# Optimization experiments

Measured on AMD Instinct MI355X. Metric: run time of the kernel, lower is better.

Reference implementation:

```python
import jax, jax.numpy as jnp
import numpy as np

B, NQ, NC, D, H = 4, 4096, 4096, 1024, 16
HD = D // H
LN_EPS = 1e-5


def _layernorm(x, g, b):
    mu = jnp.mean(x, axis=-1, keepdims=True)
    var = jnp.var(x, axis=-1, keepdims=True)
    return (x - mu) * jax.lax.rsqrt(var + LN_EPS) * g + b


def _kernel(x):
    # elu(x) + 1  (strictly positive feature map)
    return jax.nn.elu(x) + 1.0


def setup_inputs() -> dict:
    key = jax.random.key(0)
    ks = jax.random.split(key, 12)
    s = 1.0 / np.sqrt(D)
    return {
        "query": jax.random.normal(ks[0], (B, NQ, D), jnp.float32),
        "context": jax.random.normal(ks[1], (B, NC, D), jnp.float32),
        "q_w": jax.random.uniform(ks[2], (D, D), jnp.float32, -s, s),
        "q_b": jnp.zeros((D,), jnp.float32),
        "k_w": jax.random.uniform(ks[3], (D, D), jnp.float32, -s, s),
        "k_b": jnp.zeros((D,), jnp.float32),
        "v_w": jax.random.uniform(ks[4], (D, D), jnp.float32, -s, s),
        "v_b": jnp.zeros((D,), jnp.float32),
        "o_w": jax.random.uniform(ks[5], (D, D), jnp.float32, -s, s),
        "o_b": jnp.zeros((D,), jnp.float32),
        "lnq_g": jnp.ones((D,), jnp.float32),
        "lnq_b": jnp.zeros((D,), jnp.float32),
        "lnkv_g": jnp.ones((D,), jnp.float32),
        "lnkv_b": jnp.zeros((D,), jnp.float32),
    }


def reference(query, context, q_w, q_b, k_w, k_b, v_w, v_b, o_w, o_b,
              lnq_g, lnq_b, lnkv_g, lnkv_b):
    residual = query
    q = _layernorm(query, lnq_g, lnq_b)
    c = _layernorm(context, lnkv_g, lnkv_b)

    # torch Linear: y = x @ W.T + b ; reshape to (B, H, N, Hd)
    Q = (q @ q_w.T + q_b).reshape(B, NQ, H, HD).transpose(0, 2, 1, 3)
    K = (c @ k_w.T + k_b).reshape(B, NC, H, HD).transpose(0, 2, 1, 3)
    V = (c @ v_w.T + v_b).reshape(B, NC, H, HD).transpose(0, 2, 1, 3)

    Q = _kernel(Q)
    K = _kernel(K)

    # KV: (B, H, Hd, Hd) outer-product accumulation over context length
    KV = jnp.einsum("bhnd,bhne->bhde", K, V)
    K_sum = K.sum(axis=2)                              # (B, H, Hd)
    Z = jnp.einsum("bhqd,bhd->bhq", Q, K_sum)          # (B, H, Nq)
    Z = jnp.maximum(Z, 1e-6)

    out = jnp.einsum("bhqd,bhde->bhqe", Q, KV) / Z[..., None]
    out = out.transpose(0, 2, 1, 3).reshape(B, NQ, D)
    return residual + (out @ o_w.T + o_b)
```

## Files before the change

### kernel.cpp

```cpp
#include <hip/hip_runtime.h>

#define DEV __device__ __forceinline__

typedef __attribute__((ext_vector_type(8))) short short8;
typedef __attribute__((ext_vector_type(4))) short short4v;
typedef __attribute__((ext_vector_type(4))) float f32x4;

DEV float bf2f(unsigned short u) { return __uint_as_float(((unsigned int)u) << 16); }
DEV unsigned short f2bf(float f) {
    unsigned int u = __float_as_uint(f);
    u += 0x7FFFu + ((u >> 16) & 1u);
    return (unsigned short)(u >> 16);
}

DEV float elu1(float v) { return v > 0.0f ? v + 1.0f : __expf(v); }

DEV void gload_lds16(const void* g, void* l) {
    __builtin_amdgcn_global_load_lds(
        (__attribute__((address_space(1))) unsigned int*)(g),
        (__attribute__((address_space(3))) unsigned int*)(l),
        16, 0, 0);
}

#define NROW 16384
#define DDIM 1024

__global__ __launch_bounds__(256) void ln_kernel(
    const float* __restrict__ query, const float* __restrict__ context,
    const float* __restrict__ lnq_g, const float* __restrict__ lnq_b,
    const float* __restrict__ lnk_g, const float* __restrict__ lnk_b,
    unsigned short* __restrict__ qln, unsigned short* __restrict__ cln)
{
    const int row = blockIdx.x;
    const bool isq = row < NROW;
    const int r = isq ? row : row - NROW;
    const float* src = (isq ? query : context) + (size_t)r * DDIM;
    const float* g   = isq ? lnq_g : lnk_g;
    const float* bb  = isq ? lnq_b : lnk_b;
    unsigned short* dst = (isq ? qln : cln) + (size_t)r * DDIM;

    const int tid = threadIdx.x;
    f32x4 x = *(const f32x4*)(src + tid * 4);
    float s  = x[0] + x[1] + x[2] + x[3];
    float sq = x[0]*x[0] + x[1]*x[1] + x[2]*x[2] + x[3]*x[3];
#pragma unroll
    for (int off = 32; off; off >>= 1) {
        s  += __shfl_xor(s, off);
        sq += __shfl_xor(sq, off);
    }
    __shared__ float red[8];
    const int lane = tid & 63, w = tid >> 6;
    if (lane == 0) { red[w] = s; red[4 + w] = sq; }
    __syncthreads();
    s  = red[0] + red[1] + red[2] + red[3];
    sq = red[4] + red[5] + red[6] + red[7];
    const float mu  = s * (1.0f / DDIM);
    const float var = sq * (1.0f / DDIM) - mu * mu;
    const float rstd = rsqrtf(var + 1e-5f);

    f32x4 gv = *(const f32x4*)(g + tid * 4);
    f32x4 bv = *(const f32x4*)(bb + tid * 4);
    short4v o;
#pragma unroll
    for (int j = 0; j < 4; ++j)
        o[j] = (short)f2bf((x[j] - mu) * rstd * gv[j] + bv[j]);
    *(short4v*)(dst + tid * 4) = o;
}

__global__ __launch_bounds__(256) void conv_w(
    const float* __restrict__ a, const float* __restrict__ b,
    const float* __restrict__ c, const float* __restrict__ d,
    unsigned short* __restrict__ out)
{
    const int i = blockIdx.x * 256 + threadIdx.x;
    const int mat = i >> 18;
    const int idx = (i & 262143) * 4;
    const float* src = mat == 0 ? a : mat == 1 ? b : mat == 2 ? c : d;
    f32x4 v = *(const f32x4*)(src + idx);
    short4v o;
#pragma unroll
    for (int j = 0; j < 4; ++j) o[j] = (short)f2bf(v[j]);
    *(short4v*)(out + (size_t)mat * 1048576 + idx) = o;
}

template <typename EPI>
DEV void gemm128(unsigned short* __restrict__ sA,
                 unsigned short* __restrict__ sB,
                 const unsigned short* __restrict__ Ap,
                 const unsigned short* __restrict__ Bp,
                 int m0, int n0, EPI epi)
{
    const int tid = threadIdx.x;
    const int lane = tid & 63, w = tid >> 6;
    const int wr = w >> 1, wc = w & 1;
    const int lr = lane & 15, lg = lane >> 4;

    const int srow = tid >> 3;
    const int cswz = (tid & 7) ^ (srow & 7);
    const unsigned short* gA0 = Ap + (size_t)(m0 + srow) * 1024 + cswz * 8;
    const unsigned short* gB0 = Bp + (size_t)(n0 + srow) * 1024 + cswz * 8;
    unsigned short* dA = sA + tid * 8;
    unsigned short* dB = sB + tid * 8;

    const int sw0 = ((0 + lg) ^ (lr & 7)) * 8;
    const int sw1 = ((4 + lg) ^ (lr & 7)) * 8;

    f32x4 acc[4][4];
#pragma unroll
    for (int i = 0; i < 4; ++i)
#pragma unroll
        for (int j = 0; j < 4; ++j)
#pragma unroll
            for (int e = 0; e < 4; ++e) acc[i][j][e] = 0.0f;

#define STG8(T)                                                               \
    {                                                                         \
        const int ko = (T) * 64;                                              \
        _Pragma("unroll")                                                     \
        for (int j = 0; j < 4; ++j) {                                         \
            gload_lds16(gA0 + ko + (size_t)j * 32768, dA + j * 2048);         \
            gload_lds16(gB0 + ko + (size_t)j * 32768, dB + j * 2048);         \
        }                                                                     \
    }

    STG8(0);
    for (int t = 0; t < 16; ++t) {
        asm volatile("s_waitcnt vmcnt(0)" ::: "memory");
        __builtin_amdgcn_s_barrier();

        short8 af[4], bf[4];
#pragma unroll
        for (int mt = 0; mt < 4; ++mt)
            af[mt] = *(const short8*)&sA[(wr * 64 + mt * 16 + lr) * 64 + sw0];
#pragma unroll
        for (int nt = 0; nt < 4; ++nt)
            bf[nt] = *(const short8*)&sB[(wc * 64 + nt * 16 + lr) * 64 + sw0];
        __builtin_amdgcn_s_setprio(1);
#pragma unroll
        for (int mt = 0; mt < 4; ++mt)
#pragma unroll
            for (int nt = 0; nt < 4; ++nt)
                acc[mt][nt] = __builtin_amdgcn_mfma_f32_16x16x32_bf16(
                    af[mt], bf[nt], acc[mt][nt], 0, 0, 0);
        __builtin_amdgcn_s_setprio(0);

#pragma unroll
        for (int mt = 0; mt < 4; ++mt)
            af[mt] = *(const short8*)&sA[(wr * 64 + mt * 16 + lr) * 64 + sw1];
#pragma unroll
        for (int nt = 0; nt < 4; ++nt)
            bf[nt] = *(const short8*)&sB[(wc * 64 + nt * 16 + lr) * 64 + sw1];
        asm volatile("s_waitcnt lgkmcnt(0)" ::: "memory");
        __builtin_amdgcn_s_barrier();
        if (t < 15) STG8(t + 1);
        __builtin_amdgcn_s_setprio(1);
#pragma unroll
        for (int mt = 0; mt < 4; ++mt)
#pragma unroll
            for (int nt = 0; nt < 4; ++nt)
                acc[mt][nt] = __builtin_amdgcn_mfma_f32_16x16x32_bf16(
                    af[mt], bf[nt], acc[mt][nt], 0, 0, 0);
        __builtin_amdgcn_s_setprio(0);
    }
#undef STG8

#pragma unroll
    for (int mt = 0; mt < 4; ++mt)
#pragma unroll
        for (int nt = 0; nt < 4; ++nt) {
            const int col = n0 + wc * 64 + nt * 16 + lr;
#pragma unroll
            for (int i = 0; i < 4; ++i) {
                const int row = m0 + wr * 64 + mt * 16 + lg * 4 + i;
                epi(row, col, acc[mt][nt][i]);
            }
        }
}

__global__ __launch_bounds__(256, 4) void gemm_qkv(
    const unsigned short* __restrict__ QLN, const unsigned short* __restrict__ WQ,
    const unsigned short* __restrict__ CLN, const unsigned short* __restrict__ WKV,
    unsigned short* __restrict__ Qm, unsigned short* __restrict__ KVT,
    const float* __restrict__ q_b, const float* __restrict__ k_b,
    const float* __restrict__ v_b)
{
    __shared__ __attribute__((aligned(16))) unsigned short sA[128 * 64];
    __shared__ __attribute__((aligned(16))) unsigned short sB[128 * 64];

    const int bid = blockIdx.x;
    const int l = (bid & 7) * 384 + (bid >> 3);

    if (l < 1024) {
        const int m0 = (l >> 3) * 128, n0 = (l & 7) * 128;
        gemm128(sA, sB, QLN, WQ, m0, n0,
            [&](int row, int col, float v) {
                v = elu1(v + q_b[col]);
                Qm[(size_t)row * 1024 + col] = f2bf(v);
            });
    } else {
        const int r = l - 1024;
        const int m0 = (r & 15) * 128, n0 = (r >> 4) * 128;
        gemm128(sA, sB, WKV, CLN, m0, n0,
            [&](int row, int col, float v) {
                if (row < 1024) v = elu1(v + k_b[row]);
                else            v = v + v_b[row - 1024];
                KVT[(size_t)row * NROW + col] = f2bf(v);
            });
    }
}

__global__ __launch_bounds__(512, 2) void gemm_out256(
    const unsigned short* __restrict__ A, const unsigned short* __restrict__ Bm,
    float* __restrict__ Cout, const float* __restrict__ bias,
    const float* __restrict__ resid)
{
    __shared__ __attribute__((aligned(16))) unsigned short smem[65536];
    unsigned short* sAb = smem;
    unsigned short* sBb = smem + 32768;

    const int bid = blockIdx.x;
    const int l = (bid & 7) * 32 + (bid >> 3);
    const int m0 = (l >> 2) * 256, n0 = (l & 3) * 256;

    const int tid = threadIdx.x;
    const int lane = tid & 63, w = tid >> 6;
    const int wr = w >> 2, wc = w & 3;
    const int lr = lane & 15, lg = lane >> 4;

    const int srow = tid >> 3;
    const int cswz = (tid & 7) ^ (srow & 7);
    const unsigned short* gA0 = A  + (size_t)(m0 + srow) * 1024 + cswz * 8;
    const unsigned short* gB0 = Bm + (size_t)(n0 + srow) * 1024 + cswz * 8;

    const int sw0 = ((0 + lg) ^ (lr & 7)) * 8;
    const int sw1 = ((4 + lg) ^ (lr & 7)) * 8;

    f32x4 acc[8][4];
#pragma unroll
    for (int i = 0; i < 8; ++i)
#pragma unroll
        for (int j = 0; j < 4; ++j)
#pragma unroll
            for (int e = 0; e < 4; ++e) acc[i][j][e] = 0.0f;

#define STG(GP, SP, T)                                                        \
    {                                                                         \
        const unsigned short* g = (GP) + (T) * 64;                            \
        unsigned short* d = (SP) + ((T) & 1) * 16384 + tid * 8;               \
        _Pragma("unroll")                                                     \
        for (int L = 0; L < 4; ++L)                                           \
            gload_lds16(g + (size_t)L * 65536, d + L * 4096);                 \
    }

    STG(gB0, sBb, 0); STG(gA0, sAb, 0); STG(gB0, sBb, 1); STG(gA0, sAb, 1);
    asm volatile("s_waitcnt vmcnt(8)" ::: "memory");
    __builtin_amdgcn_s_barrier();

    short8 bvl[2][2];
#pragma unroll
    for (int nt = 0; nt < 2; ++nt) {
        const int rb = (wc * 64 + nt * 16 + lr) * 64;
        bvl[nt][0] = *(const short8*)&sBb[rb + sw0];
        bvl[nt][1] = *(const short8*)&sBb[rb + sw1];
    }

    for (int t = 0; t < 16; ++t) {
        const unsigned short* bA = sAb + (t & 1) * 16384;
        const unsigned short* bB = sBb + (t & 1) * 16384;
        const unsigned short* bBn = sBb + ((t + 1) & 1) * 16384;
        short8 afl[4][2], afh[4][2], bvh[2][2], bvln[2][2];

#pragma unroll
        for (int mt = 0; mt < 4; ++mt) {
            const int ra = (wr * 128 + mt * 16 + lr) * 64;
            afl[mt][0] = *(const short8*)&bA[ra + sw0];
            afl[mt][1] = *(const short8*)&bA[ra + sw1];
        }
#pragma unroll
        for (int mt = 0; mt < 4; ++mt) {
            const int ra = (wr * 128 + (mt + 4) * 16 + lr) * 64;
            afh[mt][0] = *(const short8*)&bA[ra + sw0];
            afh[mt][1] = *(const short8*)&bA[ra + sw1];
        }
        asm volatile("s_waitcnt lgkmcnt(8)" ::: "memory");
        __builtin_amdgcn_s_setprio(1);
#pragma unroll
        for (int kk = 0; kk < 2; ++kk)
#pragma unroll
            for (int mt = 0; mt < 4; ++mt)
#pragma unroll
                for (int nt = 0; nt < 2; ++nt)
                    acc[mt][nt] = __builtin_amdgcn_mfma_f32_16x16x32_bf16(
                        afl[mt][kk], bvl[nt][kk], acc[mt][nt], 0, 0, 0);
        __builtin_amdgcn_s_setprio(0);
        __builtin_amdgcn_s_barrier();

#pragma unroll
        for (int nt = 0; nt < 2; ++nt) {
            const int rb = (wc * 64 + (nt + 2) * 16 + lr) * 64;
            bvh[nt][0] = *(const short8*)&bB[rb + sw0];
            bvh[nt][1] = *(const short8*)&bB[rb + sw1];
        }
        asm volatile("s_waitcnt lgkmcnt(4)" ::: "memory");
        __builtin_amdgcn_s_setprio(1);
#pragma unroll
        for (int kk = 0; kk < 2; ++kk)
#pragma unroll
            for (int mt = 0; mt < 4; ++mt)
#pragma unroll
                for (int nt = 0; nt < 2; ++nt)
                    acc[mt + 4][nt] = __builtin_amdgcn_mfma_f32_16x16x32_bf16(
                        afh[mt][kk], bvl[nt][kk], acc[mt + 4][nt], 0, 0, 0);
        __builtin_amdgcn_s_setprio(0);
        asm volatile("s_waitcnt vmcnt(0)" ::: "memory");
        __builtin_amdgcn_s_barrier();

        if (t < 15) {
#pragma unroll
            for (int nt = 0; nt < 2; ++nt) {
                const int rb = (wc * 64 + nt * 16 + lr) * 64;
                bvln[nt][0] = *(const short8*)&bBn[rb + sw0];
                bvln[nt][1] = *(const short8*)&bBn[rb + sw1];
            }
        }
        if (t + 2 < 16) STG(gA0, sAb, t + 2);
        if (t < 15) asm volatile("s_waitcnt lgkmcnt(4)" ::: "memory");
        else        asm volatile("s_waitcnt lgkmcnt(0)" ::: "memory");
        __builtin_amdgcn_s_setprio(1);
#pragma unroll
        for (int kk = 0; kk < 2; ++kk)
#pragma unroll
            for (int mt = 0; mt < 4; ++mt)
#pragma unroll
                for (int nt = 0; nt < 2; ++nt)
                    acc[mt + 4][nt + 2] = __builtin_amdgcn_mfma_f32_16x16x32_bf16(
                        afh[mt][kk], bvh[nt][kk], acc[mt + 4][nt + 2], 0, 0, 0);
        __builtin_amdgcn_s_setprio(0);
        __builtin_amdgcn_s_barrier();

        if (t + 2 < 16) STG(gB0, sBb, t + 2);
        __builtin_amdgcn_s_setprio(1);
#pragma unroll
        for (int kk = 0; kk < 2; ++kk)
#pragma unroll
            for (int mt = 0; mt < 4; ++mt)
#pragma unroll
                for (int nt = 0; nt < 2; ++nt)
                    acc[mt][nt + 2] = __builtin_amdgcn_mfma_f32_16x16x32_bf16(
                        afl[mt][kk], bvh[nt][kk], acc[mt][nt + 2], 0, 0, 0);
        __builtin_amdgcn_s_setprio(0);

        if (t < 15) {
#pragma unroll
            for (int nt = 0; nt < 2; ++nt) {
                bvl[nt][0] = bvln[nt][0];
                bvl[nt][1] = bvln[nt][1];
            }
        }
    }
#undef STG

#pragma unroll
    for (int mt = 0; mt < 8; ++mt) {
#pragma unroll
        for (int nt = 0; nt < 4; ++nt) {
            const int col = n0 + wc * 64 + nt * 16 + lr;
#pragma unroll
            for (int i = 0; i < 4; ++i) {
                const int row = m0 + wr * 128 + mt * 16 + lg * 4 + i;
                Cout[(size_t)row * 1024 + col] =
                    acc[mt][nt][i] + bias[col] + resid[(size_t)row * 1024 + col];
            }
        }
    }
}

__global__ __launch_bounds__(256) void kv_kernel(
    const unsigned short* __restrict__ VT, const unsigned short* __restrict__ KT,
    float* __restrict__ KVTp, float* __restrict__ Ksump)
{
    const int bh = blockIdx.x, sp = blockIdx.y;
    const int b = bh >> 4, h = bh & 15;
    const int tid = threadIdx.x, lane = tid & 63, w = tid >> 6;
    const int lr = lane & 15, lg = lane >> 4;

    f32x4 acc[4][4];
#pragma unroll
    for (int i = 0; i < 4; ++i)
#pragma unroll
        for (int j = 0; j < 4; ++j)
#pragma unroll
            for (int e = 0; e < 4; ++e) acc[i][j][e] = 0.0f;
    float kp[4] = {0.0f, 0.0f, 0.0f, 0.0f};

    const size_t colbase = (size_t)b * 4096 + sp * 1024 + w * 256 + lg * 8;
    const unsigned short* va = VT + (size_t)(h * 64 + lr) * NROW + colbase;
    const unsigned short* ka = KT + (size_t)(h * 64 + lr) * NROW + colbase;

    for (int ks = 0; ks < 8; ++ks) {
        short8 af[4], bfv[4];
#pragma unroll
        for (int mt = 0; mt < 4; ++mt)
            af[mt] = *(const short8*)(va + (size_t)mt * 16 * NROW + ks * 32);
#pragma unroll
        for (int nt = 0; nt < 4; ++nt)
            bfv[nt] = *(const short8*)(ka + (size_t)nt * 16 * NROW + ks * 32);
#pragma unroll
        for (int mt = 0; mt < 4; ++mt)
#pragma unroll
            for (int nt = 0; nt < 4; ++nt)
                acc[mt][nt] = __builtin_amdgcn_mfma_f32_16x16x32_bf16(
                    af[mt], bfv[nt], acc[mt][nt], 0, 0, 0);
#pragma unroll
        for (int nt = 0; nt < 4; ++nt)
#pragma unroll
            for (int j = 0; j < 8; ++j)
                kp[nt] += bf2f((unsigned short)bfv[nt][j]);
    }

#pragma unroll
    for (int nt = 0; nt < 4; ++nt) {
        kp[nt] += __shfl_xor(kp[nt], 16);
        kp[nt] += __shfl_xor(kp[nt], 32);
    }
    __shared__ float kred[4][64];
    if (lane < 16) {
#pragma unroll
        for (int nt = 0; nt < 4; ++nt) kred[w][nt * 16 + lane] = kp[nt];
    }

    __shared__ float red4[4][4096];
#pragma unroll
    for (int mt = 0; mt < 4; ++mt)
#pragma unroll
        for (int nt = 0; nt < 4; ++nt)
#pragma unroll
            for (int i = 0; i < 4; ++i)
                red4[w][(mt * 16 + lg * 4 + i) * 64 + nt * 16 + lr] = acc[mt][nt][i];
    __syncthreads();
    float* out = KVTp + ((size_t)sp * 64 + bh) * 4096;
    for (int i = tid; i < 4096; i += 256)
        out[i] = red4[0][i] + red4[1][i] + red4[2][i] + red4[3][i];
    if (tid < 64)
        Ksump[((size_t)sp * 64 + bh) * 64 + tid] =
            kred[0][tid] + kred[1][tid] + kred[2][tid] + kred[3][tid];
}

__global__ __launch_bounds__(256) void z_kernel(
    const unsigned short* __restrict__ Q, const float* __restrict__ Ksump,
    float* __restrict__ invZ)
{
    const int gid = blockIdx.x * 256 + threadIdx.x;
    const int n = gid >> 4, h = gid & 15;
    const int b = n >> 12;
    const unsigned short* q = Q + (size_t)n * DDIM + h * 64;
    const float* k0 = Ksump + ((size_t)((b << 4) + h)) * 64;
    float z = 0.0f;
#pragma unroll
    for (int it = 0; it < 8; ++it) {
        short8 v = *(const short8*)(q + it * 8);
#pragma unroll
        for (int j = 0; j < 8; ++j) {
            const int d = it * 8 + j;
            const float ksv = k0[d] + k0[d + 4096] + k0[d + 8192] + k0[d + 12288];
            z += bf2f((unsigned short)v[j]) * ksv;
        }
    }
    invZ[gid] = 1.0f / fmaxf(z, 1e-6f);
}

__global__ __launch_bounds__(256) void a2_kernel(
    const unsigned short* __restrict__ Q, const float* __restrict__ KVTp,
    const float* __restrict__ invZ, unsigned short* __restrict__ A2)
{
    const int m0 = blockIdx.x * 128, h = blockIdx.y;
    const int b = m0 >> 12, bh = (b << 4) + h;
    const int tid = threadIdx.x, lane = tid & 63, w = tid >> 6;
    const int wr = w >> 1, wc = w & 1;
    const int lr = lane & 15, lg = lane >> 4;

    f32x4 acc[4][2];
#pragma unroll
    for (int i = 0; i < 4; ++i)
#pragma unroll
        for (int j = 0; j < 2; ++j)
#pragma unroll
            for (int e = 0; e < 4; ++e) acc[i][j][e] = 0.0f;

    const unsigned short* qa = Q + (size_t)(m0 + wr * 64 + lr) * DDIM + h * 64 + lg * 8;
    const float* kvb = KVTp + (size_t)bh * 4096 + (wc * 32 + lr) * 64 + lg * 8;

#pragma unroll
    for (int ks = 0; ks < 2; ++ks) {
        short8 af[4];
#pragma unroll
        for (int mt = 0; mt < 4; ++mt)
            af[mt] = *(const short8*)(qa + (size_t)mt * 16 * DDIM + ks * 32);
        short8 bfv[2];
#pragma unroll
        for (int nt = 0; nt < 2; ++nt) {
            const float* p = kvb + nt * 16 * 64 + ks * 32;
            short8 t;
#pragma unroll
            for (int j = 0; j < 8; ++j) {
                float v = p[j] + p[j + 262144] + p[j + 2 * 262144] + p[j + 3 * 262144];
                t[j] = (short)f2bf(v);
            }
            bfv[nt] = t;
        }
#pragma unroll
        for (int mt = 0; mt < 4; ++mt)
#pragma unroll
            for (int nt = 0; nt < 2; ++nt)
                acc[mt][nt] = __builtin_amdgcn_mfma_f32_16x16x32_bf16(
                    af[mt], bfv[nt], acc[mt][nt], 0, 0, 0);
    }

#pragma unroll
    for (int mt = 0; mt < 4; ++mt)
#pragma unroll
        for (int nt = 0; nt < 2; ++nt)
#pragma unroll
            for (int i = 0; i < 4; ++i) {
                const int row = m0 + wr * 64 + mt * 16 + lg * 4 + i;
                const int col = h * 64 + wc * 32 + nt * 16 + lr;
                const float v = acc[mt][nt][i] * invZ[row * 16 + h];
                A2[(size_t)row * DDIM + col] = f2bf(v);
            }
}

extern "C" void kernel_launch(void* const* d_in, const int* in_sizes, int n_in,
                              void* d_out, int out_size, void* d_ws, size_t ws_size,
                              hipStream_t stream)
{
    const float* query   = (const float*)d_in[0];
    const float* context = (const float*)d_in[1];
    const float* q_w = (const float*)d_in[2];
    const float* q_b = (const float*)d_in[3];
    const float* k_w = (const float*)d_in[4];
    const float* k_b = (const float*)d_in[5];
    const float* v_w = (const float*)d_in[6];
    const float* v_b = (const float*)d_in[7];
    const float* o_w = (const float*)d_in[8];
    const float* o_b = (const float*)d_in[9];
    const float* lnq_g = (const float*)d_in[10];
    const float* lnq_b = (const float*)d_in[11];
    const float* lnk_g = (const float*)d_in[12];
    const float* lnk_b = (const float*)d_in[13];

    char* ws = (char*)d_ws;
    unsigned short* WQ  = (unsigned short*)(ws);
    unsigned short* WKV = (unsigned short*)(ws + (2u << 20));
    unsigned short* WO  = (unsigned short*)(ws + (6u << 20));
    unsigned short* QLN = (unsigned short*)(ws + (8u << 20));
    unsigned short* CLN = (unsigned short*)(ws + (40u << 20));
    unsigned short* Qm  = (unsigned short*)(ws + (72u << 20));
    unsigned short* KT  = (unsigned short*)(ws + (104u << 20));
    unsigned short* VT  = (unsigned short*)(ws + (136u << 20));
    float* KVTp  = (float*)(ws + (168u << 20));
    float* Ksump = (float*)(ws + (172u << 20));
    float* invZ  = (float*)(ws + (173u << 20));
    unsigned short* A2 = QLN;

    conv_w<<<4096, 256, 0, stream>>>(q_w, k_w, v_w, o_w, WQ);
    ln_kernel<<<2 * NROW, 256, 0, stream>>>(query, context, lnq_g, lnq_b,
                                            lnk_g, lnk_b, QLN, CLN);
    gemm_qkv<<<3072, 256, 0, stream>>>(QLN, WQ, CLN, WKV, Qm, KT,
                                       q_b, k_b, v_b);
    kv_kernel<<<dim3(64, 4), 256, 0, stream>>>(VT, KT, KVTp, Ksump);
    z_kernel<<<1024, 256, 0, stream>>>(Qm, Ksump, invZ);
    a2_kernel<<<dim3(128, 16), 256, 0, stream>>>(Qm, KVTp, invZ, A2);
    gemm_out256<<<256, 512, 0, stream>>>(A2, WO, (float*)d_out, o_b, query);
}
```

Before: 316.9 us.

## Fuse weight conversion into LN, Z into a2, and split KV over more blocks

Folds the weight bf16 conversion into the layernorm launch as extra blocks and removes the separate z_kernel. The normalizer Z is now computed inside a2_kernel from the Q fragments it already loads plus an LDS copy of the summed K. kv_kernel's context split goes from 4 to 8 chunks, launching 512 blocks instead of 256 for better occupancy. The cost is that a2 must reduce 8 partial KV tiles per element instead of 4, and the workspace offsets are adjusted to fit the larger partial buffer.

```diff
diff --git a/kernel.cpp b/kernel.cpp
--- a/kernel.cpp
+++ b/kernel.cpp
@@ -29,8 +29,25 @@
     const float* __restrict__ query, const float* __restrict__ context,
     const float* __restrict__ lnq_g, const float* __restrict__ lnq_b,
     const float* __restrict__ lnk_g, const float* __restrict__ lnk_b,
-    unsigned short* __restrict__ qln, unsigned short* __restrict__ cln)
-{
+    unsigned short* __restrict__ qln, unsigned short* __restrict__ cln,
+    const float* __restrict__ q_w, const float* __restrict__ k_w,
+    const float* __restrict__ v_w, const float* __restrict__ o_w,
+    unsigned short* __restrict__ wout)
+{
+    const int tid = threadIdx.x;
+    if (blockIdx.x >= 2 * NROW) {
+        const int i = (blockIdx.x - 2 * NROW) * 256 + tid;
+        const int mat = i >> 18;
+        const int idx = (i & 262143) * 4;
+        const float* src = mat == 0 ? q_w : mat == 1 ? k_w : mat == 2 ? v_w : o_w;
+        f32x4 v = *(const f32x4*)(src + idx);
+        short4v o;
+#pragma unroll
+        for (int j = 0; j < 4; ++j) o[j] = (short)f2bf(v[j]);
+        *(short4v*)(wout + (size_t)mat * 1048576 + idx) = o;
+        return;
+    }
+
     const int row = blockIdx.x;
     const bool isq = row < NROW;
     const int r = isq ? row : row - NROW;
@@ -39,7 +56,6 @@
     const float* bb  = isq ? lnq_b : lnk_b;
     unsigned short* dst = (isq ? qln : cln) + (size_t)r * DDIM;
 
-    const int tid = threadIdx.x;
     f32x4 x = *(const f32x4*)(src + tid * 4);
     float s  = x[0] + x[1] + x[2] + x[3];
     float sq = x[0]*x[0] + x[1]*x[1] + x[2]*x[2] + x[3]*x[3];
@@ -65,22 +81,6 @@
     for (int j = 0; j < 4; ++j)
         o[j] = (short)f2bf((x[j] - mu) * rstd * gv[j] + bv[j]);
     *(short4v*)(dst + tid * 4) = o;
-}
-
-__global__ __launch_bounds__(256) void conv_w(
-    const float* __restrict__ a, const float* __restrict__ b,
-    const float* __restrict__ c, const float* __restrict__ d,
-    unsigned short* __restrict__ out)
-{
-    const int i = blockIdx.x * 256 + threadIdx.x;
-    const int mat = i >> 18;
-    const int idx = (i & 262143) * 4;
-    const float* src = mat == 0 ? a : mat == 1 ? b : mat == 2 ? c : d;
-    f32x4 v = *(const f32x4*)(src + idx);
-    short4v o;
-#pragma unroll
-    for (int j = 0; j < 4; ++j) o[j] = (short)f2bf(v[j]);
-    *(short4v*)(out + (size_t)mat * 1048576 + idx) = o;
 }
 
 template <typename EPI>
@@ -393,11 +393,11 @@
             for (int e = 0; e < 4; ++e) acc[i][j][e] = 0.0f;
     float kp[4] = {0.0f, 0.0f, 0.0f, 0.0f};
 
-    const size_t colbase = (size_t)b * 4096 + sp * 1024 + w * 256 + lg * 8;
+    const size_t colbase = (size_t)b * 4096 + sp * 512 + w * 128 + lg * 8;
     const unsigned short* va = VT + (size_t)(h * 64 + lr) * NROW + colbase;
     const unsigned short* ka = KT + (size_t)(h * 64 + lr) * NROW + colbase;
 
-    for (int ks = 0; ks < 8; ++ks) {
+    for (int ks = 0; ks < 4; ++ks) {
         short8 af[4], bfv[4];
 #pragma unroll
         for (int mt = 0; mt < 4; ++mt)
@@ -446,32 +446,9 @@
             kred[0][tid] + kred[1][tid] + kred[2][tid] + kred[3][tid];
 }
 
-__global__ __launch_bounds__(256) void z_kernel(
-    const unsigned short* __restrict__ Q, const float* __restrict__ Ksump,
-    float* __restrict__ invZ)
-{
-    const int gid = blockIdx.x * 256 + threadIdx.x;
-    const int n = gid >> 4, h = gid & 15;
-    const int b = n >> 12;
-    const unsigned short* q = Q + (size_t)n * DDIM + h * 64;
-    const float* k0 = Ksump + ((size_t)((b << 4) + h)) * 64;
-    float z = 0.0f;
-#pragma unroll
-    for (int it = 0; it < 8; ++it) {
-        short8 v = *(const short8*)(q + it * 8);
-#pragma unroll
-        for (int j = 0; j < 8; ++j) {
-            const int d = it * 8 + j;
-            const float ksv = k0[d] + k0[d + 4096] + k0[d + 8192] + k0[d + 12288];
-            z += bf2f((unsigned short)v[j]) * ksv;
-        }
-    }
-    invZ[gid] = 1.0f / fmaxf(z, 1e-6f);
-}
-
 __global__ __launch_bounds__(256) void a2_kernel(
     const unsigned short* __restrict__ Q, const float* __restrict__ KVTp,
-    const float* __restrict__ invZ, unsigned short* __restrict__ A2)
+    const float* __restrict__ Ksump, unsigned short* __restrict__ A2)
 {
     const int m0 = blockIdx.x * 128, h = blockIdx.y;
     const int b = m0 >> 12, bh = (b << 4) + h;
@@ -479,6 +456,16 @@
     const int wr = w >> 1, wc = w & 1;
     const int lr = lane & 15, lg = lane >> 4;
 
+    __shared__ float ksum_s[64];
+    if (tid < 64) {
+        float s = 0.0f;
+#pragma unroll
+        for (int sp = 0; sp < 8; ++sp)
+            s += Ksump[((size_t)sp * 64 + bh) * 64 + tid];
+        ksum_s[tid] = s;
+    }
+    __syncthreads();
+
     f32x4 acc[4][2];
 #pragma unroll
     for (int i = 0; i < 4; ++i)
@@ -486,6 +473,7 @@
         for (int j = 0; j < 2; ++j)
 #pragma unroll
             for (int e = 0; e < 4; ++e) acc[i][j][e] = 0.0f;
+    float zp[4] = {0.0f, 0.0f, 0.0f, 0.0f};
 
     const unsigned short* qa = Q + (size_t)(m0 + wr * 64 + lr) * DDIM + h * 64 + lg * 8;
     const float* kvb = KVTp + (size_t)bh * 4096 + (wc * 32 + lr) * 64 + lg * 8;
@@ -496,6 +484,11 @@
 #pragma unroll
         for (int mt = 0; mt < 4; ++mt)
             af[mt] = *(const short8*)(qa + (size_t)mt * 16 * DDIM + ks * 32);
+#pragma unroll
+        for (int mt = 0; mt < 4; ++mt)
+#pragma unroll
+            for (int j = 0; j < 8; ++j)
+                zp[mt] += bf2f((unsigned short)af[mt][j]) * ksum_s[ks * 32 + lg * 8 + j];
         short8 bfv[2];
 #pragma unroll
         for (int nt = 0; nt < 2; ++nt) {
@@ -503,7 +496,9 @@
             short8 t;
 #pragma unroll
             for (int j = 0; j < 8; ++j) {
-                float v = p[j] + p[j + 262144] + p[j + 2 * 262144] + p[j + 3 * 262144];
+                float v = 0.0f;
+#pragma unroll
+                for (int sp = 0; sp < 8; ++sp) v += p[j + sp * 262144];
                 t[j] = (short)f2bf(v);
             }
             bfv[nt] = t;
@@ -516,6 +511,14 @@
                     af[mt], bfv[nt], acc[mt][nt], 0, 0, 0);
     }
 
+    float zinv[4];
+#pragma unroll
+    for (int mt = 0; mt < 4; ++mt) {
+        zp[mt] += __shfl_xor(zp[mt], 16);
+        zp[mt] += __shfl_xor(zp[mt], 32);
+        zinv[mt] = 1.0f / fmaxf(zp[mt], 1e-6f);
+    }
+
 #pragma unroll
     for (int mt = 0; mt < 4; ++mt)
 #pragma unroll
@@ -524,7 +527,8 @@
             for (int i = 0; i < 4; ++i) {
                 const int row = m0 + wr * 64 + mt * 16 + lg * 4 + i;
                 const int col = h * 64 + wc * 32 + nt * 16 + lr;
-                const float v = acc[mt][nt][i] * invZ[row * 16 + h];
+                const float zi = __shfl(zinv[mt], lg * 4 + i);
+                const float v = acc[mt][nt][i] * zi;
                 A2[(size_t)row * DDIM + col] = f2bf(v);
             }
 }
@@ -558,17 +562,15 @@
     unsigned short* KT  = (unsigned short*)(ws + (104u << 20));
     unsigned short* VT  = (unsigned short*)(ws + (136u << 20));
     float* KVTp  = (float*)(ws + (168u << 20));
-    float* Ksump = (float*)(ws + (172u << 20));
-    float* invZ  = (float*)(ws + (173u << 20));
+    float* Ksump = (float*)(ws + (176u << 20));
     unsigned short* A2 = QLN;
 
-    conv_w<<<4096, 256, 0, stream>>>(q_w, k_w, v_w, o_w, WQ);
-    ln_kernel<<<2 * NROW, 256, 0, stream>>>(query, context, lnq_g, lnq_b,
-                                            lnk_g, lnk_b, QLN, CLN);
+    ln_kernel<<<2 * NROW + 4096, 256, 0, stream>>>(
+        query, context, lnq_g, lnq_b, lnk_g, lnk_b, QLN, CLN,
+        q_w, k_w, v_w, o_w, WQ);
     gemm_qkv<<<3072, 256, 0, stream>>>(QLN, WQ, CLN, WKV, Qm, KT,
                                        q_b, k_b, v_b);
-    kv_kernel<<<dim3(64, 4), 256, 0, stream>>>(VT, KT, KVTp, Ksump);
-    z_kernel<<<1024, 256, 0, stream>>>(Qm, Ksump, invZ);
-    a2_kernel<<<dim3(128, 16), 256, 0, stream>>>(Qm, KVTp, invZ, A2);
+    kv_kernel<<<dim3(64, 8), 256, 0, stream>>>(VT, KT, KVTp, Ksump);
+    a2_kernel<<<dim3(128, 16), 256, 0, stream>>>(Qm, KVTp, Ksump, A2);
     gemm_out256<<<256, 512, 0, stream>>>(A2, WO, (float*)d_out, o_b, query);
 }
```

Result: no change. 318.4 us (+0.5%).
